# Kernel tuning notes

Measured on AMD Instinct MI355X. Metric: run time of the kernel, lower is better.

The kernel has to match this reference:

```python
import jax, jax.numpy as jnp
import numpy as np

N_EMBED = 1024
HEAD_COUNT = 16
HEAD_SIZE = 64  # HEAD_COUNT * HEAD_SIZE == N_EMBED
SEQ = 2048
BATCH = 2


def setup_inputs() -> dict:
    key = jax.random.key(0)
    k_ix, k_q, k_k, k_v, k_p, k_b = jax.random.split(key, 6)
    scale = 1.0 / np.sqrt(N_EMBED)
    inp = {
        "ix": jax.random.normal(k_ix, (BATCH, SEQ, N_EMBED), dtype=jnp.float32),
        # per-head projection weights, stored as x @ W form: [H, C, D]
        "Wq": jax.random.normal(k_q, (HEAD_COUNT, N_EMBED, HEAD_SIZE), dtype=jnp.float32) * scale,
        "Wk": jax.random.normal(k_k, (HEAD_COUNT, N_EMBED, HEAD_SIZE), dtype=jnp.float32) * scale,
        "Wv": jax.random.normal(k_v, (HEAD_COUNT, N_EMBED, HEAD_SIZE), dtype=jnp.float32) * scale,
        # output projection (Linear with bias): y = x @ Wp + bp
        "Wp": jax.random.normal(k_p, (N_EMBED, N_EMBED), dtype=jnp.float32) * scale,
        "bp": jax.random.normal(k_b, (N_EMBED,), dtype=jnp.float32) * scale,
    }
    return inp


def reference(ix, Wq, Wk, Wv, Wp, bp):
    B, T, C = ix.shape
    # per-head projections: [B, H, T, D]
    Q = jnp.einsum("btc,hcd->bhtd", ix, Wq)
    K = jnp.einsum("btc,hcd->bhtd", ix, Wk)
    V = jnp.einsum("btc,hcd->bhtd", ix, Wv)
    # NOTE: faithful to source -- scores are MULTIPLIED by sqrt(C) (C = n_embed)
    scores = jnp.einsum("bhtd,bhsd->bhts", Q, K) * (C ** 0.5)
    causal = jnp.tril(jnp.ones((T, T), dtype=bool))
    scores = jnp.where(causal, scores, -jnp.inf)
    wei = jax.nn.softmax(scores, axis=-1)
    out = jnp.einsum("bhts,bhsd->bhtd", wei, V)
    # concat heads (matches torch.cat over per-head outputs along last dim)
    out = out.transpose(0, 2, 1, 3).reshape(B, T, -1)
    return out @ Wp + bp
```

## Files before the change

### kernel.cpp

```cpp
#include <hip/hip_runtime.h>

#define BATCH 2
#define SEQL  2048
#define NEMB  1024
#define NH    16
#define HD    64
#define MROWS (BATCH*SEQL)

typedef short bf16x8 __attribute__((ext_vector_type(8)));
typedef float f32x16 __attribute__((ext_vector_type(16)));

__device__ __forceinline__ unsigned short f2bf(float x) {
    union { float f; unsigned u; } v; v.f = x;
    unsigned r = v.u + 0x7FFFu + ((v.u >> 16) & 1u);
    return (unsigned short)(r >> 16);
}
__device__ __forceinline__ void split_bf16(float x, unsigned short& hi, unsigned short& lo) {
    hi = f2bf(x);
    union { unsigned u; float f; } h; h.u = ((unsigned)hi) << 16;
    lo = f2bf(x - h.f);
}

__device__ __forceinline__ int slot16(int chunk, int lane) {
    return chunk * 66 + (lane & 31) + 33 * (lane >> 5);
}

__global__ __launch_bounds__(256) void split_convert_kernel(
    const float* __restrict__ src,
    unsigned short* __restrict__ dhi, unsigned short* __restrict__ dlo)
{
    int i = (blockIdx.x * 256 + threadIdx.x) * 4;
    float4 v = *(const float4*)(src + i);
    unsigned short h[4], l[4];
    split_bf16(v.x, h[0], l[0]); split_bf16(v.y, h[1], l[1]);
    split_bf16(v.z, h[2], l[2]); split_bf16(v.w, h[3], l[3]);
    uint2 ph, pl;
    ph.x = h[0] | ((unsigned)h[1] << 16); ph.y = h[2] | ((unsigned)h[3] << 16);
    pl.x = l[0] | ((unsigned)l[1] << 16); pl.y = l[2] | ((unsigned)l[3] << 16);
    *(uint2*)(dhi + i) = ph;
    *(uint2*)(dlo + i) = pl;
}

__global__ __launch_bounds__(256) void transpose_convert_kernel(
    const float* __restrict__ Wq, const float* __restrict__ Wk,
    const float* __restrict__ Wv, const float* __restrict__ Wp,
    unsigned short* __restrict__ qhi, unsigned short* __restrict__ qlo,
    unsigned short* __restrict__ khi, unsigned short* __restrict__ klo,
    unsigned short* __restrict__ vhi, unsigned short* __restrict__ pt)
{
    __shared__ float tile[64][68];
    const int z = blockIdx.z, hb = blockIdx.y, c0 = blockIdx.x * 64;
    const float* src; int rstride; unsigned short* dhi; unsigned short* dlo;
    if (z == 0)      { src = Wq + (size_t)hb * 65536; rstride = 64;   dhi = qhi; dlo = qlo; }
    else if (z == 1) { src = Wk + (size_t)hb * 65536; rstride = 64;   dhi = khi; dlo = klo; }
    else if (z == 2) { src = Wv + (size_t)hb * 65536; rstride = 64;   dhi = vhi; dlo = nullptr; }
    else             { src = Wp + (size_t)hb * 64;    rstride = 1024; dhi = pt;  dlo = nullptr; }
    const int tid = threadIdx.x;
    #pragma unroll
    for (int i = 0; i < 4; ++i) {
        int fidx = i * 256 + tid;
        int r  = fidx >> 4;
        int dq = (fidx & 15) * 4;
        float4 v = *(const float4*)(src + (size_t)(c0 + r) * rstride + dq);
        *(float4*)&tile[r][dq] = v;
    }
    __syncthreads();
    #pragma unroll
    for (int i = 0; i < 4; ++i) {
        int fidx = i * 256 + tid;
        int d  = fidx >> 4;
        int cq = (fidx & 15) * 4;
        size_t base = (size_t)(hb * 64 + d) * 1024 + c0 + cq;
        unsigned short hh[4], ll[4];
        #pragma unroll
        for (int j = 0; j < 4; ++j) split_bf16(tile[cq + j][d], hh[j], ll[j]);
        uint2 ph; ph.x = hh[0] | ((unsigned)hh[1] << 16); ph.y = hh[2] | ((unsigned)hh[3] << 16);
        *(uint2*)(dhi + base) = ph;
        if (dlo) {
            uint2 pl; pl.x = ll[0] | ((unsigned)ll[1] << 16); pl.y = ll[2] | ((unsigned)ll[3] << 16);
            *(uint2*)(dlo + base) = pl;
        }
    }
}

__global__ __launch_bounds__(256, 2) void qkv_gemm(
    const unsigned short* __restrict__ Ahi, const unsigned short* __restrict__ Alo,
    const unsigned short* __restrict__ Bq_hi, const unsigned short* __restrict__ Bq_lo,
    const unsigned short* __restrict__ Bk_hi, const unsigned short* __restrict__ Bk_lo,
    const unsigned short* __restrict__ Bv_hi,
    unsigned short* __restrict__ Qhi, unsigned short* __restrict__ Qlo,
    unsigned short* __restrict__ Khi, unsigned short* __restrict__ Klo,
    unsigned short* __restrict__ Vt)
{
    __shared__ unsigned short smem[2][4][4224];

    const int z = blockIdx.z;
    const bool split = (z < 2);
    const unsigned short* __restrict__ Bhi = (z == 0) ? Bq_hi : (z == 1) ? Bk_hi : Bv_hi;
    const unsigned short* __restrict__ Blo = (z == 0) ? Bq_lo : Bk_lo;
    unsigned short* __restrict__ Ohi = (z == 0) ? Qhi : Khi;
    unsigned short* __restrict__ Olo = (z == 0) ? Qlo : Klo;
    const float oscale = (z == 0) ? 32.0f : 1.0f;

    const int m0 = blockIdx.x * 128;
    const int n0 = blockIdx.y * 128;
    const int tid  = threadIdx.x;
    const int wid  = tid >> 6, lane = tid & 63;
    const int wr   = wid >> 1, wc = wid & 1;

    int roff_[2], slot_[2];
    #pragma unroll
    for (int q = 0; q < 2; ++q) {
        int f   = q * 256 + tid;
        int row = f >> 2;
        int k8  = (f & 3) * 8;
        roff_[q] = row * 1024 + k8;
        slot_[q] = slot16((row >> 5) * 2 + (k8 >> 4), (row & 31) + 32 * ((k8 >> 3) & 1)) * 8;
    }
    const unsigned short* __restrict__ Ah = Ahi + (size_t)m0 * 1024;
    const unsigned short* __restrict__ Bh = Bhi + (size_t)n0 * 1024;
    const unsigned short* __restrict__ Al = split ? Alo + (size_t)m0 * 1024 : Ahi;
    const unsigned short* __restrict__ Bl = split ? Blo + (size_t)n0 * 1024 : Bhi;

    bf16x8 pah[2], pbh[2], pal[2], pbl[2];

    #define LOADT(KK)  do { _Pragma("unroll")                                   \
        for (int q = 0; q < 2; ++q) {                                           \
            pah[q] = *(const bf16x8*)(Ah + roff_[q] + (KK));                    \
            pbh[q] = *(const bf16x8*)(Bh + roff_[q] + (KK));                    \
            if (split) {                                                        \
                pal[q] = *(const bf16x8*)(Al + roff_[q] + (KK));                \
                pbl[q] = *(const bf16x8*)(Bl + roff_[q] + (KK));                \
            }                                                                   \
        } } while (0)

    #define WRITET(NB) do { _Pragma("unroll")                                   \
        for (int q = 0; q < 2; ++q) {                                           \
            *(bf16x8*)(&smem[NB][0][slot_[q]]) = pah[q];                        \
            *(bf16x8*)(&smem[NB][1][slot_[q]]) = pbh[q];                        \
            if (split) {                                                        \
                *(bf16x8*)(&smem[NB][2][slot_[q]]) = pal[q];                    \
                *(bf16x8*)(&smem[NB][3][slot_[q]]) = pbl[q];                    \
            }                                                                   \
        } } while (0)

    f32x16 acc[2][2] = {};

    LOADT(0);
    WRITET(0);
    LOADT(32);

    for (int t = 0; t < 32; ++t) {
        __syncthreads();
        if (t + 1 < 32) {
            WRITET((t + 1) & 1);
            if (t + 2 < 32) LOADT((t + 2) * 32);
        }
        const int cb = t & 1;
        const unsigned short* a_hi = smem[cb][0];
        const unsigned short* b_hi = smem[cb][1];
        const unsigned short* a_lo = smem[cb][2];
        const unsigned short* b_lo = smem[cb][3];

        #pragma unroll
        for (int kch = 0; kch < 2; ++kch) {
            bf16x8 ah[2], bh_[2];
            #pragma unroll
            for (int mt = 0; mt < 2; ++mt)
                ah[mt] = *(const bf16x8*)(a_hi + slot16((2 * wr + mt) * 2 + kch, lane) * 8);
            #pragma unroll
            for (int nt = 0; nt < 2; ++nt)
                bh_[nt] = *(const bf16x8*)(b_hi + slot16((2 * wc + nt) * 2 + kch, lane) * 8);
            if (split) {
                bf16x8 al[2], bl[2];
                #pragma unroll
                for (int mt = 0; mt < 2; ++mt)
                    al[mt] = *(const bf16x8*)(a_lo + slot16((2 * wr + mt) * 2 + kch, lane) * 8);
                #pragma unroll
                for (int nt = 0; nt < 2; ++nt)
                    bl[nt] = *(const bf16x8*)(b_lo + slot16((2 * wc + nt) * 2 + kch, lane) * 8);
                #pragma unroll
                for (int mt = 0; mt < 2; ++mt)
                    #pragma unroll
                    for (int nt = 0; nt < 2; ++nt) {
                        acc[mt][nt] = __builtin_amdgcn_mfma_f32_32x32x16_bf16(ah[mt], bh_[nt], acc[mt][nt], 0, 0, 0);
                        acc[mt][nt] = __builtin_amdgcn_mfma_f32_32x32x16_bf16(ah[mt], bl[nt],  acc[mt][nt], 0, 0, 0);
                        acc[mt][nt] = __builtin_amdgcn_mfma_f32_32x32x16_bf16(al[mt], bh_[nt], acc[mt][nt], 0, 0, 0);
                    }
            } else {
                #pragma unroll
                for (int mt = 0; mt < 2; ++mt)
                    #pragma unroll
                    for (int nt = 0; nt < 2; ++nt)
                        acc[mt][nt] = __builtin_amdgcn_mfma_f32_32x32x16_bf16(bh_[nt], ah[mt], acc[mt][nt], 0, 0, 0);
            }
        }
    }
    #undef LOADT
    #undef WRITET

    #pragma unroll
    for (int mt = 0; mt < 2; ++mt) {
        #pragma unroll
        for (int nt = 0; nt < 2; ++nt) {
            if (z == 2) {
                const int mcol = m0 + wr * 64 + mt * 32 + (lane & 31);
                const int bb = mcol >> 11, tt = mcol & (SEQL - 1);
                #pragma unroll
                for (int r = 0; r < 16; ++r) {
                    int nrow = n0 + wc * 64 + nt * 32 + (r & 3) + 8 * (r >> 2) + 4 * (lane >> 5);
                    int head = nrow >> 6, dd = nrow & 63;
                    Vt[((size_t)(bb * NH + head) * HD + dd) * SEQL + tt] = f2bf(acc[mt][nt][r]);
                }
            } else {
                const int ncol = n0 + wc * 64 + nt * 32 + (lane & 31);
                const int head = ncol >> 6, d = ncol & 63;
                #pragma unroll
                for (int r = 0; r < 16; ++r) {
                    int mrow = m0 + wr * 64 + mt * 32 + (r & 3) + 8 * (r >> 2) + 4 * (lane >> 5);
                    int bb = mrow >> 11, t = mrow & (SEQL - 1);
                    size_t idx = ((size_t)(bb * NH + head) * SEQL + t) * HD + d;
                    float v = acc[mt][nt][r] * oscale;
                    unsigned short hi = f2bf(v);
                    Ohi[idx] = hi;
                    union { unsigned u; float f; } hf; hf.u = ((unsigned)hi) << 16;
                    Olo[idx] = f2bf(v - hf.f);
                }
            }
        }
    }
}

__global__ __launch_bounds__(256) void attn_mfma_kernel(
    const unsigned short* __restrict__ Qhi, const unsigned short* __restrict__ Qlo,
    const unsigned short* __restrict__ Khi, const unsigned short* __restrict__ Klo,
    const unsigned short* __restrict__ Vt,
    unsigned short* __restrict__ AO)
{
    __shared__ unsigned short smem[2][3][4224];

    const int bid = blockIdx.x;
    const int xcd = bid & 7;
    const int idx = bid >> 3;
    const int bh  = xcd * 4 + (idx & 3);
    const int g   = 15 - (idx >> 2);

    const int tid  = threadIdx.x;
    const int wid  = tid >> 6;
    const int lane = tid & 63;
    const int ln   = lane & 31;
    const int h    = lane >> 5;

    const int qb_idx = g * 4 + wid;
    const int qb     = qb_idx * 32;
    const int qglob  = qb + ln;
    const int my_nt  = (qb_idx >> 1) + 1;
    const int tmax   = 2 * g + 2;

    const unsigned short* __restrict__ Qbh = Qhi + (size_t)bh * SEQL * HD;
    const unsigned short* __restrict__ Qbl = Qlo + (size_t)bh * SEQL * HD;
    const unsigned short* __restrict__ Kbh = Khi + (size_t)bh * SEQL * HD;
    const unsigned short* __restrict__ Kbl = Klo + (size_t)bh * SEQL * HD;
    const unsigned short* __restrict__ Vtb = Vt  + (size_t)bh * HD * SEQL;

    bf16x8 qhi[4], qlo[4];
    #pragma unroll
    for (int c = 0; c < 4; ++c) {
        qhi[c] = *(const bf16x8*)(Qbh + (size_t)qglob * HD + c * 16 + h * 8);
        qlo[c] = *(const bf16x8*)(Qbl + (size_t)qglob * HD + c * 16 + h * 8);
    }

    int s_[2], d8_[2], ks_[2];
    #pragma unroll
    for (int ff = 0; ff < 2; ++ff) {
        int fidx = ff * 256 + tid;
        s_[ff]  = fidx >> 3;
        d8_[ff] = fidx & 7;
        ks_[ff] = slot16((s_[ff] >> 5) * 4 + (d8_[ff] >> 1),
                         (s_[ff] & 31) + 32 * (d8_[ff] & 1)) * 8;
    }

    bf16x8 kh[2], kl[2], vv[2];
    #pragma unroll
    for (int ff = 0; ff < 2; ++ff) {
        kh[ff] = *(const bf16x8*)(Kbh + (size_t)s_[ff] * HD + d8_[ff] * 8);
        kl[ff] = *(const bf16x8*)(Kbl + (size_t)s_[ff] * HD + d8_[ff] * 8);
        vv[ff] = *(const bf16x8*)(Vtb + (size_t)s_[ff] * SEQL + d8_[ff] * 8);
    }
    #pragma unroll
    for (int ff = 0; ff < 2; ++ff) {
        *(bf16x8*)(&smem[0][0][ks_[ff]]) = kh[ff];
        *(bf16x8*)(&smem[0][1][ks_[ff]]) = kl[ff];
        *(bf16x8*)(&smem[0][2][ks_[ff]]) = vv[ff];
    }
    if (tmax > 1) {
        #pragma unroll
        for (int ff = 0; ff < 2; ++ff) {
            kh[ff] = *(const bf16x8*)(Kbh + (size_t)(64 + s_[ff]) * HD + d8_[ff] * 8);
            kl[ff] = *(const bf16x8*)(Kbl + (size_t)(64 + s_[ff]) * HD + d8_[ff] * 8);
            vv[ff] = *(const bf16x8*)(Vtb + (size_t)s_[ff] * SEQL + 64 + d8_[ff] * 8);
        }
    }

    f32x16 oacc[2] = {};
    float m_run = -1e30f, l_run = 0.f;

    for (int t = 0; t < tmax; ++t) {
        __syncthreads();
        if (t + 1 < tmax) {
            const int nb = (t + 1) & 1;
            #pragma unroll
            for (int ff = 0; ff < 2; ++ff) {
                *(bf16x8*)(&smem[nb][0][ks_[ff]]) = kh[ff];
                *(bf16x8*)(&smem[nb][1][ks_[ff]]) = kl[ff];
                *(bf16x8*)(&smem[nb][2][ks_[ff]]) = vv[ff];
            }
            if (t + 2 < tmax) {
                const int s0n = (t + 2) * 64;
                #pragma unroll
                for (int ff = 0; ff < 2; ++ff) {
                    kh[ff] = *(const bf16x8*)(Kbh + (size_t)(s0n + s_[ff]) * HD + d8_[ff] * 8);
                    kl[ff] = *(const bf16x8*)(Kbl + (size_t)(s0n + s_[ff]) * HD + d8_[ff] * 8);
                    vv[ff] = *(const bf16x8*)(Vtb + (size_t)s_[ff] * SEQL + s0n + d8_[ff] * 8);
                }
            }
        }

        if (t < my_nt) {
            const int cb = t & 1;
            const int s0 = t * 64;
            const bf16x8* khf = (const bf16x8*)&smem[cb][0][0];
            const bf16x8* klf = (const bf16x8*)&smem[cb][1][0];
            const bf16x8* vtf = (const bf16x8*)&smem[cb][2][0];

            f32x16 sacc[2] = {};
            __builtin_amdgcn_s_setprio(1);
            #pragma unroll
            for (int sb = 0; sb < 2; ++sb) {
                #pragma unroll
                for (int c = 0; c < 4; ++c) {
                    bf16x8 ah = khf[slot16(sb * 4 + c, lane)];
                    bf16x8 al = klf[slot16(sb * 4 + c, lane)];
                    sacc[sb] = __builtin_amdgcn_mfma_f32_32x32x16_bf16(ah, qhi[c], sacc[sb], 0, 0, 0);
                    sacc[sb] = __builtin_amdgcn_mfma_f32_32x32x16_bf16(ah, qlo[c], sacc[sb], 0, 0, 0);
                    sacc[sb] = __builtin_amdgcn_mfma_f32_32x32x16_bf16(al, qhi[c], sacc[sb], 0, 0, 0);
                }
            }
            __builtin_amdgcn_s_setprio(0);

            const bool diag = (s0 + 63) > qb;
            float mtile = -1e30f;
            #pragma unroll
            for (int sb = 0; sb < 2; ++sb) {
                #pragma unroll
                for (int r = 0; r < 16; ++r) {
                    int srow = (r & 3) + 8 * (r >> 2) + 4 * h + sb * 32;
                    float x = sacc[sb][r];
                    if (diag && (s0 + srow) > qglob) x = -1e30f;
                    sacc[sb][r] = x;
                    mtile = fmaxf(mtile, x);
                }
            }
            mtile = fmaxf(mtile, __shfl_xor(mtile, 32));
            const float mnew  = fmaxf(m_run, mtile);
            const float alpha = __expf(m_run - mnew);

            float psum = 0.f;
            unsigned pw[2][8];
            #pragma unroll
            for (int sb = 0; sb < 2; ++sb) {
                #pragma unroll
                for (int r2 = 0; r2 < 8; ++r2) {
                    float p0 = __expf(sacc[sb][2 * r2]     - mnew);
                    float p1 = __expf(sacc[sb][2 * r2 + 1] - mnew);
                    psum += p0 + p1;
                    pw[sb][r2] = (unsigned)f2bf(p0) | ((unsigned)f2bf(p1) << 16);
                }
            }
            psum += __shfl_xor(psum, 32);
            l_run = l_run * alpha + psum;
            m_run = mnew;
            #pragma unroll
            for (int dt = 0; dt < 2; ++dt)
                #pragma unroll
                for (int r = 0; r < 16; ++r)
                    oacc[dt][r] *= alpha;

            unsigned px[2][8];
            #pragma unroll
            for (int sb = 0; sb < 2; ++sb)
                #pragma unroll
                for (int i = 0; i < 8; ++i)
                    px[sb][i] = __shfl_xor(pw[sb][i], 32);

            bf16x8 pfrag[4];
            #pragma unroll
            for (int sb = 0; sb < 2; ++sb) {
                #pragma unroll
                for (int c = 0; c < 2; ++c) {
                    unsigned u0, u1, u2, u3;
                    if (h == 0) { u0 = pw[sb][4*c];   u1 = pw[sb][4*c+1]; u2 = px[sb][4*c];   u3 = px[sb][4*c+1]; }
                    else        { u0 = px[sb][4*c+2]; u1 = px[sb][4*c+3]; u2 = pw[sb][4*c+2]; u3 = pw[sb][4*c+3]; }
                    union { unsigned u[4]; bf16x8 v; } cvt;
                    cvt.u[0] = u0; cvt.u[1] = u1; cvt.u[2] = u2; cvt.u[3] = u3;
                    pfrag[sb * 2 + c] = cvt.v;
                }
            }

            __builtin_amdgcn_s_setprio(1);
            #pragma unroll
            for (int dt = 0; dt < 2; ++dt)
                #pragma unroll
                for (int sc = 0; sc < 4; ++sc)
                    oacc[dt] = __builtin_amdgcn_mfma_f32_32x32x16_bf16(
                        vtf[slot16(dt * 4 + sc, lane)], pfrag[sc], oacc[dt], 0, 0, 0);
            __builtin_amdgcn_s_setprio(0);
        }
    }

    const float inv = 1.0f / l_run;
    unsigned short* aop = AO + ((size_t)(bh >> 4) * SEQL + qglob) * NEMB + (bh & 15) * HD;
    #pragma unroll
    for (int dt = 0; dt < 2; ++dt) {
        #pragma unroll
        for (int rg = 0; rg < 4; ++rg) {
            int d0 = dt * 32 + rg * 8 + h * 4;
            unsigned short b0 = f2bf(oacc[dt][rg * 4 + 0] * inv);
            unsigned short b1 = f2bf(oacc[dt][rg * 4 + 1] * inv);
            unsigned short b2 = f2bf(oacc[dt][rg * 4 + 2] * inv);
            unsigned short b3 = f2bf(oacc[dt][rg * 4 + 3] * inv);
            uint2 w;
            w.x = (unsigned)b0 | ((unsigned)b1 << 16);
            w.y = (unsigned)b2 | ((unsigned)b3 << 16);
            *(uint2*)(aop + d0) = w;
        }
    }
}

__global__ __launch_bounds__(256, 2) void out_proj_kernel(
    const unsigned short* __restrict__ A, const unsigned short* __restrict__ B,
    const float* __restrict__ bias, float* __restrict__ out)
{
    __shared__ unsigned short smem[2][2][4224];

    const int m0 = blockIdx.x * 128;
    const int n0 = blockIdx.y * 128;
    const int tid  = threadIdx.x;
    const int wid  = tid >> 6, lane = tid & 63;
    const int wr   = wid >> 1, wc = wid & 1;

    int roff_[2], slot_[2];
    #pragma unroll
    for (int q = 0; q < 2; ++q) {
        int f   = q * 256 + tid;
        int row = f >> 2;
        int k8  = (f & 3) * 8;
        roff_[q] = row * 1024 + k8;
        slot_[q] = slot16((row >> 5) * 2 + (k8 >> 4), (row & 31) + 32 * ((k8 >> 3) & 1)) * 8;
    }
    const unsigned short* __restrict__ Ab = A + (size_t)m0 * 1024;
    const unsigned short* __restrict__ Bb = B + (size_t)n0 * 1024;

    bf16x8 pa[2], pb[2];
    #pragma unroll
    for (int q = 0; q < 2; ++q) {
        pa[q] = *(const bf16x8*)(Ab + roff_[q]);
        pb[q] = *(const bf16x8*)(Bb + roff_[q]);
    }
    #pragma unroll
    for (int q = 0; q < 2; ++q) {
        *(bf16x8*)(&smem[0][0][slot_[q]]) = pa[q];
        *(bf16x8*)(&smem[0][1][slot_[q]]) = pb[q];
    }
    #pragma unroll
    for (int q = 0; q < 2; ++q) {
        pa[q] = *(const bf16x8*)(Ab + roff_[q] + 32);
        pb[q] = *(const bf16x8*)(Bb + roff_[q] + 32);
    }

    f32x16 acc[2][2] = {};

    for (int t = 0; t < 32; ++t) {
        __syncthreads();
        if (t + 1 < 32) {
            const int nb = (t + 1) & 1;
            #pragma unroll
            for (int q = 0; q < 2; ++q) {
                *(bf16x8*)(&smem[nb][0][slot_[q]]) = pa[q];
                *(bf16x8*)(&smem[nb][1][slot_[q]]) = pb[q];
            }
            if (t + 2 < 32) {
                #pragma unroll
                for (int q = 0; q < 2; ++q) {
                    pa[q] = *(const bf16x8*)(Ab + roff_[q] + (t + 2) * 32);
                    pb[q] = *(const bf16x8*)(Bb + roff_[q] + (t + 2) * 32);
                }
            }
        }
        const int cb = t & 1;
        const unsigned short* a_s = smem[cb][0];
        const unsigned short* b_s = smem[cb][1];
        #pragma unroll
        for (int kch = 0; kch < 2; ++kch) {
            bf16x8 ah[2], bh_[2];
            #pragma unroll
            for (int mt = 0; mt < 2; ++mt)
                ah[mt] = *(const bf16x8*)(a_s + slot16((2 * wr + mt) * 2 + kch, lane) * 8);
            #pragma unroll
            for (int nt = 0; nt < 2; ++nt)
                bh_[nt] = *(const bf16x8*)(b_s + slot16((2 * wc + nt) * 2 + kch, lane) * 8);
            #pragma unroll
            for (int mt = 0; mt < 2; ++mt)
                #pragma unroll
                for (int nt = 0; nt < 2; ++nt)
                    acc[mt][nt] = __builtin_amdgcn_mfma_f32_32x32x16_bf16(ah[mt], bh_[nt], acc[mt][nt], 0, 0, 0);
        }
    }

    #pragma unroll
    for (int mt = 0; mt < 2; ++mt) {
        #pragma unroll
        for (int nt = 0; nt < 2; ++nt) {
            const int ncol = n0 + wc * 64 + nt * 32 + (lane & 31);
            const float bv = bias[ncol];
            #pragma unroll
            for (int r = 0; r < 16; ++r) {
                int mrow = m0 + wr * 64 + mt * 32 + (r & 3) + 8 * (r >> 2) + 4 * (lane >> 5);
                out[(size_t)mrow * 1024 + ncol] = acc[mt][nt][r] + bv;
            }
        }
    }
}

extern "C" void kernel_launch(void* const* d_in, const int* in_sizes, int n_in,
                              void* d_out, int out_size, void* d_ws, size_t ws_size,
                              hipStream_t stream)
{
    const float* ix = (const float*)d_in[0];
    const float* Wq = (const float*)d_in[1];
    const float* Wk = (const float*)d_in[2];
    const float* Wv = (const float*)d_in[3];
    const float* Wp = (const float*)d_in[4];
    const float* bp = (const float*)d_in[5];
    float* out = (float*)d_out;

    char* ws = (char*)d_ws;
    #define WSOFF(mb) ((unsigned short*)(ws + (size_t)(mb) * 1024 * 1024))
    unsigned short* ix_hi  = WSOFF(0);
    unsigned short* ix_lo  = WSOFF(8);
    unsigned short* Wqt_hi = WSOFF(16);
    unsigned short* Wqt_lo = WSOFF(18);
    unsigned short* Wkt_hi = WSOFF(20);
    unsigned short* Wkt_lo = WSOFF(22);
    unsigned short* Wvt_hi = WSOFF(24);
    unsigned short* Qhi    = WSOFF(26);
    unsigned short* Qlo    = WSOFF(34);
    unsigned short* Khi    = WSOFF(42);
    unsigned short* Klo    = WSOFF(50);
    unsigned short* Wpt    = WSOFF(58);
    unsigned short* AObf   = WSOFF(0);
    unsigned short* Vt     = (unsigned short*)d_out;
    #undef WSOFF

    split_convert_kernel<<<MROWS * NEMB / 4 / 256, 256, 0, stream>>>(ix, ix_hi, ix_lo);
    transpose_convert_kernel<<<dim3(16, 16, 4), 256, 0, stream>>>(
        Wq, Wk, Wv, Wp, Wqt_hi, Wqt_lo, Wkt_hi, Wkt_lo, Wvt_hi, Wpt);
    qkv_gemm<<<dim3(MROWS / 128, NEMB / 128, 3), 256, 0, stream>>>(
        ix_hi, ix_lo, Wqt_hi, Wqt_lo, Wkt_hi, Wkt_lo, Wvt_hi,
        Qhi, Qlo, Khi, Klo, Vt);
    attn_mfma_kernel<<<512, 256, 0, stream>>>(Qhi, Qlo, Khi, Klo, Vt, AObf);
    out_proj_kernel<<<dim3(MROWS / 128, NEMB / 128), 256, 0, stream>>>(AObf, Wpt, bp, out);
}
```

Before: 193.4 us.

## Drop LDS staging in attention, use exp2 with lazy rescale and packed bf16 converts

```diff
diff --git a/kernel.cpp b/kernel.cpp
--- a/kernel.cpp
+++ b/kernel.cpp
@@ -7,6 +7,8 @@
 #define HD    64
 #define MROWS (BATCH*SEQL)
 
+#define QSCALE 46.166241308446828f
+
 typedef short bf16x8 __attribute__((ext_vector_type(8)));
 typedef float f32x16 __attribute__((ext_vector_type(16)));
 
@@ -19,6 +21,11 @@
     hi = f2bf(x);
     union { unsigned u; float f; } h; h.u = ((unsigned)hi) << 16;
     lo = f2bf(x - h.f);
+}
+__device__ __forceinline__ unsigned cvt_pk_bf16(float a, float b) {
+    unsigned r;
+    asm("v_cvt_pk_bf16_f32 %0, %1, %2" : "=v"(r) : "v"(a), "v"(b));
+    return r;
 }
 
 __device__ __forceinline__ int slot16(int chunk, int lane) {
@@ -100,7 +107,7 @@
     const unsigned short* __restrict__ Blo = (z == 0) ? Bq_lo : Bk_lo;
     unsigned short* __restrict__ Ohi = (z == 0) ? Qhi : Khi;
     unsigned short* __restrict__ Olo = (z == 0) ? Qlo : Klo;
-    const float oscale = (z == 0) ? 32.0f : 1.0f;
+    const float oscale = (z == 0) ? QSCALE : 1.0f;
 
     const int m0 = blockIdx.x * 128;
     const int n0 = blockIdx.y * 128;
@@ -231,19 +238,17 @@
     }
 }
 
-__global__ __launch_bounds__(256) void attn_mfma_kernel(
+__global__ __launch_bounds__(256, 3) void attn_mfma_kernel(
     const unsigned short* __restrict__ Qhi, const unsigned short* __restrict__ Qlo,
     const unsigned short* __restrict__ Khi, const unsigned short* __restrict__ Klo,
     const unsigned short* __restrict__ Vt,
     unsigned short* __restrict__ AO)
 {
-    __shared__ unsigned short smem[2][3][4224];
-
     const int bid = blockIdx.x;
     const int xcd = bid & 7;
     const int idx = bid >> 3;
     const int bh  = xcd * 4 + (idx & 3);
-    const int g   = 15 - (idx >> 2);
+    const int j   = idx >> 2;
 
     const int tid  = threadIdx.x;
     const int wid  = tid >> 6;
@@ -251,11 +256,10 @@
     const int ln   = lane & 31;
     const int h    = lane >> 5;
 
-    const int qb_idx = g * 4 + wid;
+    const int qb_idx = (15 - j) * 4 + wid;
     const int qb     = qb_idx * 32;
     const int qglob  = qb + ln;
-    const int my_nt  = (qb_idx >> 1) + 1;
-    const int tmax   = 2 * g + 2;
+    const int ntiles = (qb_idx >> 1) + 1;
 
     const unsigned short* __restrict__ Qbh = Qhi + (size_t)bh * SEQL * HD;
     const unsigned short* __restrict__ Qbl = Qlo + (size_t)bh * SEQL * HD;
@@ -270,152 +274,106 @@
         qlo[c] = *(const bf16x8*)(Qbl + (size_t)qglob * HD + c * 16 + h * 8);
     }
 
-    int s_[2], d8_[2], ks_[2];
-    #pragma unroll
-    for (int ff = 0; ff < 2; ++ff) {
-        int fidx = ff * 256 + tid;
-        s_[ff]  = fidx >> 3;
-        d8_[ff] = fidx & 7;
-        ks_[ff] = slot16((s_[ff] >> 5) * 4 + (d8_[ff] >> 1),
-                         (s_[ff] & 31) + 32 * (d8_[ff] & 1)) * 8;
-    }
-
-    bf16x8 kh[2], kl[2], vv[2];
-    #pragma unroll
-    for (int ff = 0; ff < 2; ++ff) {
-        kh[ff] = *(const bf16x8*)(Kbh + (size_t)s_[ff] * HD + d8_[ff] * 8);
-        kl[ff] = *(const bf16x8*)(Kbl + (size_t)s_[ff] * HD + d8_[ff] * 8);
-        vv[ff] = *(const bf16x8*)(Vtb + (size_t)s_[ff] * SEQL + d8_[ff] * 8);
-    }
-    #pragma unroll
-    for (int ff = 0; ff < 2; ++ff) {
-        *(bf16x8*)(&smem[0][0][ks_[ff]]) = kh[ff];
-        *(bf16x8*)(&smem[0][1][ks_[ff]]) = kl[ff];
-        *(bf16x8*)(&smem[0][2][ks_[ff]]) = vv[ff];
-    }
-    if (tmax > 1) {
-        #pragma unroll
-        for (int ff = 0; ff < 2; ++ff) {
-            kh[ff] = *(const bf16x8*)(Kbh + (size_t)(64 + s_[ff]) * HD + d8_[ff] * 8);
-            kl[ff] = *(const bf16x8*)(Kbl + (size_t)(64 + s_[ff]) * HD + d8_[ff] * 8);
-            vv[ff] = *(const bf16x8*)(Vtb + (size_t)s_[ff] * SEQL + 64 + d8_[ff] * 8);
-        }
-    }
+    const size_t koff = (size_t)ln * HD + h * 8;
+    const size_t voff = (size_t)ln * SEQL + h * 8;
 
     f32x16 oacc[2] = {};
     float m_run = -1e30f, l_run = 0.f;
 
-    for (int t = 0; t < tmax; ++t) {
-        __syncthreads();
-        if (t + 1 < tmax) {
-            const int nb = (t + 1) & 1;
-            #pragma unroll
-            for (int ff = 0; ff < 2; ++ff) {
-                *(bf16x8*)(&smem[nb][0][ks_[ff]]) = kh[ff];
-                *(bf16x8*)(&smem[nb][1][ks_[ff]]) = kl[ff];
-                *(bf16x8*)(&smem[nb][2][ks_[ff]]) = vv[ff];
-            }
-            if (t + 2 < tmax) {
-                const int s0n = (t + 2) * 64;
-                #pragma unroll
-                for (int ff = 0; ff < 2; ++ff) {
-                    kh[ff] = *(const bf16x8*)(Kbh + (size_t)(s0n + s_[ff]) * HD + d8_[ff] * 8);
-                    kl[ff] = *(const bf16x8*)(Kbl + (size_t)(s0n + s_[ff]) * HD + d8_[ff] * 8);
-                    vv[ff] = *(const bf16x8*)(Vtb + (size_t)s_[ff] * SEQL + s0n + d8_[ff] * 8);
-                }
-            }
-        }
-
-        if (t < my_nt) {
-            const int cb = t & 1;
-            const int s0 = t * 64;
-            const bf16x8* khf = (const bf16x8*)&smem[cb][0][0];
-            const bf16x8* klf = (const bf16x8*)&smem[cb][1][0];
-            const bf16x8* vtf = (const bf16x8*)&smem[cb][2][0];
-
-            f32x16 sacc[2] = {};
-            __builtin_amdgcn_s_setprio(1);
-            #pragma unroll
-            for (int sb = 0; sb < 2; ++sb) {
-                #pragma unroll
-                for (int c = 0; c < 4; ++c) {
-                    bf16x8 ah = khf[slot16(sb * 4 + c, lane)];
-                    bf16x8 al = klf[slot16(sb * 4 + c, lane)];
-                    sacc[sb] = __builtin_amdgcn_mfma_f32_32x32x16_bf16(ah, qhi[c], sacc[sb], 0, 0, 0);
-                    sacc[sb] = __builtin_amdgcn_mfma_f32_32x32x16_bf16(ah, qlo[c], sacc[sb], 0, 0, 0);
-                    sacc[sb] = __builtin_amdgcn_mfma_f32_32x32x16_bf16(al, qhi[c], sacc[sb], 0, 0, 0);
-                }
-            }
-            __builtin_amdgcn_s_setprio(0);
-
-            const bool diag = (s0 + 63) > qb;
-            float mtile = -1e30f;
-            #pragma unroll
-            for (int sb = 0; sb < 2; ++sb) {
-                #pragma unroll
-                for (int r = 0; r < 16; ++r) {
-                    int srow = (r & 3) + 8 * (r >> 2) + 4 * h + sb * 32;
-                    float x = sacc[sb][r];
-                    if (diag && (s0 + srow) > qglob) x = -1e30f;
-                    sacc[sb][r] = x;
-                    mtile = fmaxf(mtile, x);
-                }
-            }
-            mtile = fmaxf(mtile, __shfl_xor(mtile, 32));
+    for (int t = 0; t < ntiles; ++t) {
+        const int s0 = t * 64;
+        const unsigned short* __restrict__ kb_h = Kbh + (size_t)s0 * HD + koff;
+        const unsigned short* __restrict__ kb_l = Kbl + (size_t)s0 * HD + koff;
+
+        f32x16 sacc[2] = {};
+        __builtin_amdgcn_s_setprio(1);
+        #pragma unroll
+        for (int sb = 0; sb < 2; ++sb) {
+            #pragma unroll
+            for (int c = 0; c < 4; ++c) {
+                bf16x8 ah = *(const bf16x8*)(kb_h + sb * 32 * HD + c * 16);
+                bf16x8 al = *(const bf16x8*)(kb_l + sb * 32 * HD + c * 16);
+                sacc[sb] = __builtin_amdgcn_mfma_f32_32x32x16_bf16(ah, qhi[c], sacc[sb], 0, 0, 0);
+                sacc[sb] = __builtin_amdgcn_mfma_f32_32x32x16_bf16(ah, qlo[c], sacc[sb], 0, 0, 0);
+                sacc[sb] = __builtin_amdgcn_mfma_f32_32x32x16_bf16(al, qhi[c], sacc[sb], 0, 0, 0);
+            }
+        }
+        __builtin_amdgcn_s_setprio(0);
+
+        const bool diag = (s0 + 63) > qb;
+        float mtile = -1e30f;
+        #pragma unroll
+        for (int sb = 0; sb < 2; ++sb) {
+            #pragma unroll
+            for (int r = 0; r < 16; ++r) {
+                int srow = (r & 3) + 8 * (r >> 2) + 4 * h + sb * 32;
+                float x = sacc[sb][r];
+                if (diag && (s0 + srow) > qglob) x = -1e30f;
+                sacc[sb][r] = x;
+                mtile = fmaxf(mtile, x);
+            }
+        }
+        mtile = fmaxf(mtile, __shfl_xor(mtile, 32));
+
+        if (!__all(mtile - m_run <= 11.5f)) {
             const float mnew  = fmaxf(m_run, mtile);
-            const float alpha = __expf(m_run - mnew);
-
-            float psum = 0.f;
-            unsigned pw[2][8];
-            #pragma unroll
-            for (int sb = 0; sb < 2; ++sb) {
-                #pragma unroll
-                for (int r2 = 0; r2 < 8; ++r2) {
-                    float p0 = __expf(sacc[sb][2 * r2]     - mnew);
-                    float p1 = __expf(sacc[sb][2 * r2 + 1] - mnew);
-                    psum += p0 + p1;
-                    pw[sb][r2] = (unsigned)f2bf(p0) | ((unsigned)f2bf(p1) << 16);
-                }
-            }
-            psum += __shfl_xor(psum, 32);
-            l_run = l_run * alpha + psum;
-            m_run = mnew;
+            const float alpha = exp2f(m_run - mnew);
+            l_run *= alpha;
             #pragma unroll
             for (int dt = 0; dt < 2; ++dt)
                 #pragma unroll
                 for (int r = 0; r < 16; ++r)
                     oacc[dt][r] *= alpha;
-
-            unsigned px[2][8];
-            #pragma unroll
-            for (int sb = 0; sb < 2; ++sb)
-                #pragma unroll
-                for (int i = 0; i < 8; ++i)
-                    px[sb][i] = __shfl_xor(pw[sb][i], 32);
-
-            bf16x8 pfrag[4];
-            #pragma unroll
-            for (int sb = 0; sb < 2; ++sb) {
-                #pragma unroll
-                for (int c = 0; c < 2; ++c) {
-                    unsigned u0, u1, u2, u3;
-                    if (h == 0) { u0 = pw[sb][4*c];   u1 = pw[sb][4*c+1]; u2 = px[sb][4*c];   u3 = px[sb][4*c+1]; }
-                    else        { u0 = px[sb][4*c+2]; u1 = px[sb][4*c+3]; u2 = pw[sb][4*c+2]; u3 = pw[sb][4*c+3]; }
-                    union { unsigned u[4]; bf16x8 v; } cvt;
-                    cvt.u[0] = u0; cvt.u[1] = u1; cvt.u[2] = u2; cvt.u[3] = u3;
-                    pfrag[sb * 2 + c] = cvt.v;
-                }
-            }
-
-            __builtin_amdgcn_s_setprio(1);
-            #pragma unroll
-            for (int dt = 0; dt < 2; ++dt)
-                #pragma unroll
-                for (int sc = 0; sc < 4; ++sc)
-                    oacc[dt] = __builtin_amdgcn_mfma_f32_32x32x16_bf16(
-                        vtf[slot16(dt * 4 + sc, lane)], pfrag[sc], oacc[dt], 0, 0, 0);
-            __builtin_amdgcn_s_setprio(0);
-        }
+            m_run = mnew;
+        }
+
+        float psum = 0.f;
+        unsigned pw[2][8];
+        #pragma unroll
+        for (int sb = 0; sb < 2; ++sb) {
+            #pragma unroll
+            for (int r2 = 0; r2 < 8; ++r2) {
+                float p0 = exp2f(sacc[sb][2 * r2]     - m_run);
+                float p1 = exp2f(sacc[sb][2 * r2 + 1] - m_run);
+                psum += p0 + p1;
+                pw[sb][r2] = cvt_pk_bf16(p0, p1);
+            }
+        }
+        psum += __shfl_xor(psum, 32);
+        l_run += psum;
+
+        unsigned px[2][8];
+        #pragma unroll
+        for (int sb = 0; sb < 2; ++sb)
+            #pragma unroll
+            for (int i = 0; i < 8; ++i)
+                px[sb][i] = __shfl_xor(pw[sb][i], 32);
+
+        bf16x8 pfrag[4];
+        #pragma unroll
+        for (int sb = 0; sb < 2; ++sb) {
+            #pragma unroll
+            for (int c = 0; c < 2; ++c) {
+                unsigned u0, u1, u2, u3;
+                if (h == 0) { u0 = pw[sb][4*c];   u1 = pw[sb][4*c+1]; u2 = px[sb][4*c];   u3 = px[sb][4*c+1]; }
+                else        { u0 = px[sb][4*c+2]; u1 = px[sb][4*c+3]; u2 = pw[sb][4*c+2]; u3 = pw[sb][4*c+3]; }
+                union { unsigned u[4]; bf16x8 v; } cvt;
+                cvt.u[0] = u0; cvt.u[1] = u1; cvt.u[2] = u2; cvt.u[3] = u3;
+                pfrag[sb * 2 + c] = cvt.v;
+            }
+        }
+
+        __builtin_amdgcn_s_setprio(1);
+        #pragma unroll
+        for (int dt = 0; dt < 2; ++dt) {
+            const unsigned short* __restrict__ vb = Vtb + (size_t)dt * 32 * SEQL + voff + s0;
+            #pragma unroll
+            for (int sc = 0; sc < 4; ++sc) {
+                bf16x8 vf = *(const bf16x8*)(vb + sc * 16);
+                oacc[dt] = __builtin_amdgcn_mfma_f32_32x32x16_bf16(vf, pfrag[sc], oacc[dt], 0, 0, 0);
+            }
+        }
+        __builtin_amdgcn_s_setprio(0);
     }
 
     const float inv = 1.0f / l_run;
@@ -425,13 +383,9 @@
         #pragma unroll
         for (int rg = 0; rg < 4; ++rg) {
             int d0 = dt * 32 + rg * 8 + h * 4;
-            unsigned short b0 = f2bf(oacc[dt][rg * 4 + 0] * inv);
-            unsigned short b1 = f2bf(oacc[dt][rg * 4 + 1] * inv);
-            unsigned short b2 = f2bf(oacc[dt][rg * 4 + 2] * inv);
-            unsigned short b3 = f2bf(oacc[dt][rg * 4 + 3] * inv);
             uint2 w;
-            w.x = (unsigned)b0 | ((unsigned)b1 << 16);
-            w.y = (unsigned)b2 | ((unsigned)b3 << 16);
+            w.x = cvt_pk_bf16(oacc[dt][rg * 4 + 0] * inv, oacc[dt][rg * 4 + 1] * inv);
+            w.y = cvt_pk_bf16(oacc[dt][rg * 4 + 2] * inv, oacc[dt][rg * 4 + 3] * inv);
             *(uint2*)(aop + d0) = w;
         }
     }
```

After: 251.3 us. 30.0% more time.
